# Optimization experiments

Measured on AMD Instinct MI355X. Metric: run time of the kernel, lower is better.

The kernel has to match this reference:

```python
import jax, jax.numpy as jnp
import numpy as np
import math

D_MODEL = 1024
NUM_HEADS = 16
D_K = D_MODEL // NUM_HEADS
B, S = 2, 2048


def _linear_weight(key, out_f, in_f):
    return jax.random.normal(key, (out_f, in_f), jnp.float32) * math.sqrt(2.0 / in_f)


def setup_inputs() -> dict:
    key = jax.random.key(0)
    ks = jax.random.split(key, 5)
    x = jax.random.normal(ks[0], (B, S, D_MODEL), jnp.float32)
    return {
        "x": x,
        "Wq": _linear_weight(ks[1], D_MODEL, D_MODEL),
        "bq": jnp.zeros((D_MODEL,), jnp.float32),
        "Wk": _linear_weight(ks[2], D_MODEL, D_MODEL),
        "bk": jnp.zeros((D_MODEL,), jnp.float32),
        "Wv": _linear_weight(ks[3], D_MODEL, D_MODEL),
        "bv": jnp.zeros((D_MODEL,), jnp.float32),
        "Wo": _linear_weight(ks[4], D_MODEL, D_MODEL),
        "bo": jnp.zeros((D_MODEL,), jnp.float32),
    }


def reference(x, Wq, bq, Wk, bk, Wv, bv, Wo, bo):
    b, s, _ = x.shape
    # Projections: x @ W.T + b (CustomLinear stores weight as (out, in))
    q = jnp.einsum("bsd,ed->bse", x, Wq) + bq
    k = jnp.einsum("bsd,ed->bse", x, Wk) + bk
    v = jnp.einsum("bsd,ed->bse", x, Wv) + bv
    # (b, h, s, d_k)
    q = q.reshape(b, s, NUM_HEADS, D_K).transpose(0, 2, 1, 3)
    k = k.reshape(b, s, NUM_HEADS, D_K).transpose(0, 2, 1, 3)
    v = v.reshape(b, s, NUM_HEADS, D_K).transpose(0, 2, 1, 3)
    # Scaled dot-product attention with fully materialized scores (faithful)
    scores = jnp.einsum("bhqd,bhkd->bhqk", q, k) / math.sqrt(D_K)
    attn = jax.nn.softmax(scores, axis=-1)
    out = jnp.einsum("bhqk,bhkd->bhqd", attn, v)
    out = out.transpose(0, 2, 1, 3).reshape(b, s, D_MODEL)
    return jnp.einsum("bsd,ed->bse", out, Wo) + bo
```

## Files before the change

kernel.cpp:

```cpp
#include <hip/hip_runtime.h>
#include <hip/hip_bf16.h>

using bf16 = __hip_bfloat16;
typedef __attribute__((ext_vector_type(8))) short short8;
typedef __attribute__((ext_vector_type(4))) short s4v;
typedef __attribute__((ext_vector_type(4))) float float4v;
typedef __attribute__((ext_vector_type(4))) float f32x4;

#define MFMA16(a, b, c) __builtin_amdgcn_mfma_f32_16x16x32_bf16((a), (b), (c), 0, 0, 0)

#define GLD_LDS16(g, l)                                            \
    __builtin_amdgcn_global_load_lds(                              \
        (const __attribute__((address_space(1))) void*)(g),        \
        (__attribute__((address_space(3))) void*)(l), 16, 0, 0)

constexpr int Bc = 2;
constexpr int Sc = 2048;
constexpr int Hc = 16;
constexpr int DKc = 64;
constexpr int Dc = 1024;
constexpr size_t MEG = 1024 * 1024;

union BFU { bf16 h; short s; };

__device__ inline short bfbits(float f) {
    BFU u; u.h = __float2bfloat16(f); return u.s;
}

__device__ inline float bits2f(short s) {
    BFU u; u.s = s; return __bfloat162float(u.h);
}

__device__ inline short8 load_cvt8(const float* __restrict__ p) {
    f32x4 a = *(const f32x4*)p;
    f32x4 b = *(const f32x4*)(p + 4);
    short8 r;
    r[0] = bfbits(a[0]); r[1] = bfbits(a[1]); r[2] = bfbits(a[2]); r[3] = bfbits(a[3]);
    r[4] = bfbits(b[0]); r[5] = bfbits(b[1]); r[6] = bfbits(b[2]); r[7] = bfbits(b[3]);
    return r;
}

__global__ __launch_bounds__(256) void cvt_kernel(
    const float* __restrict__ x, const float* __restrict__ Wq,
    const float* __restrict__ Wk, const float* __restrict__ Wv,
    const float* __restrict__ Wo, bf16* __restrict__ dst)
{
    const size_t i = ((size_t)blockIdx.x * 256 + threadIdx.x) * 8;
    const float* s;
    if      (i < 4 * MEG) s = x  + i;
    else if (i < 5 * MEG) s = Wq + (i - 4 * MEG);
    else if (i < 6 * MEG) s = Wk + (i - 5 * MEG);
    else if (i < 7 * MEG) s = Wv + (i - 6 * MEG);
    else                  s = Wo + (i - 7 * MEG);
    *(short8*)(dst + i) = load_cvt8(s);
}

__global__ __launch_bounds__(256) void qkv_gemm_kernel(
    const bf16* __restrict__ x,
    const bf16* __restrict__ Wq, const float* __restrict__ bq,
    const bf16* __restrict__ Wk, const float* __restrict__ bk,
    const bf16* __restrict__ Wv, const float* __restrict__ bv,
    bf16* __restrict__ q_ws, bf16* __restrict__ k_ws, bf16* __restrict__ v_ws)
{
    constexpr int BM = 128, BN = 128, BK = 32;
    __shared__ __align__(16) bf16 sA[BM * BK];
    __shared__ __align__(16) bf16 sB[BN * BK];

    const int bx = blockIdx.x;
    const int sel = bx >> 3;
    const int n0 = (bx & 7) * BN;
    const int m0 = blockIdx.y * BM;

    const bf16* __restrict__ Wsel = (sel == 0) ? Wq : ((sel == 1) ? Wk : Wv);
    const float* __restrict__ bsel = (sel == 0) ? bq : ((sel == 1) ? bk : bv);

    const int t = threadIdx.x;
    const int lane = t & 63;
    const int wave = t >> 6;
    const int ln = lane & 15;
    const int qd = lane >> 4;
    const int wm = (wave >> 1) * 64;
    const int wn = (wave & 1) * 64;

    const int gr = lane >> 2;
    const int gc = (lane & 3) * 8;

    float4v acc[4][4];
#pragma unroll
    for (int i = 0; i < 4; i++)
#pragma unroll
        for (int j = 0; j < 4; j++) acc[i][j] = (float4v)0.0f;

    for (int kk = 0; kk < Dc; kk += BK) {
        __syncthreads();
#pragma unroll
        for (int cc = 0; cc < 2; cc++) {
            const int c = wave * 2 + cc;
            GLD_LDS16(x    + (size_t)(m0 + c * 16 + gr) * Dc + kk + gc, &sA[c * 512]);
            GLD_LDS16(Wsel + (size_t)(n0 + c * 16 + gr) * Dc + kk + gc, &sB[c * 512]);
        }
        __syncthreads();

        short8 af[4], wf[4];
#pragma unroll
        for (int i = 0; i < 4; i++)
            af[i] = *(const short8*)&sA[(wm + i * 16 + ln) * BK + qd * 8];
#pragma unroll
        for (int j = 0; j < 4; j++)
            wf[j] = *(const short8*)&sB[(wn + j * 16 + ln) * BK + qd * 8];
#pragma unroll
        for (int i = 0; i < 4; i++)
#pragma unroll
            for (int j = 0; j < 4; j++)
                acc[i][j] = MFMA16(af[i], wf[j], acc[i][j]);
    }

    constexpr float QSCALE = 0.125f * 1.44269504088896f;

#pragma unroll
    for (int j = 0; j < 4; j++) {
        const int n = n0 + wn + j * 16 + ln;
        const float bias = bsel[n];
        const int h_ = n >> 6, d_ = n & 63;
#pragma unroll
        for (int i = 0; i < 4; i++) {
            const int mbase = m0 + wm + i * 16 + qd * 4;
            if (sel == 2) {
                const int b_ = mbase >> 11, s_ = mbase & 2047;
                s4v pk;
#pragma unroll
                for (int r = 0; r < 4; r++)
                    pk[r] = bfbits(acc[i][j][r] + bias);
                *(s4v*)&v_ws[(((size_t)(b_ * Hc + h_)) * DKc + d_) * Sc + s_] = pk;
            } else {
#pragma unroll
                for (int r = 0; r < 4; r++) {
                    const int m = mbase + r;
                    const int b_ = m >> 11, s_ = m & 2047;
                    float v = acc[i][j][r] + bias;
                    if (sel == 0) v *= QSCALE;
                    const bf16 o = __float2bfloat16(v);
                    if (sel == 0)
                        q_ws[(((size_t)(b_ * Hc + h_)) * Sc + s_) * DKc + d_] = o;
                    else
                        k_ws[(((size_t)(b_ * Hc + h_)) * Sc + s_) * DKc + d_] = o;
                }
            }
        }
    }
}

__global__ __launch_bounds__(512, 6) void attn_kernel(
    const bf16* __restrict__ q_ws, const bf16* __restrict__ k_ws,
    const bf16* __restrict__ v_ws, bf16* __restrict__ po0,
    bf16* __restrict__ po1, float* __restrict__ l_ws)
{
    constexpr int LQP = 76;
    constexpr int NKT = 16;
    __shared__ __align__(16) bf16 sK[2][64 * 64];
    __shared__ __align__(16) bf16 sV[2][64 * 64];
    __shared__ __align__(16) short sP[8][16 * LQP];

    const int bh = blockIdx.x;
    const int qt = blockIdx.y;
    const int sp = blockIdx.z;
    const int t = threadIdx.x;
    const int lane = t & 63;
    const int wave = t >> 6;
    const int ln = lane & 15;
    const int qd = lane >> 4;
    short* const sPw = sP[wave];

    const bf16* __restrict__ Qbase = q_ws + (size_t)bh * Sc * DKc + qt * 128 * DKc;
    const bf16* __restrict__ Kbase = k_ws + ((size_t)bh * Sc + sp * 1024) * DKc;
    const bf16* __restrict__ Vbase = v_ws + (size_t)bh * DKc * Sc + sp * 1024;

    const int rloc = lane >> 3;
    const int blk = lane & 7;

    short8 qf[2];
#pragma unroll
    for (int ks = 0; ks < 2; ks++)
        qf[ks] = *(const short8*)
            (Qbase + (size_t)(wave * 16 + ln) * DKc + ks * 32 + qd * 8);

    {
        const int row = wave * 8 + rloc;
        const int gb = blk ^ (row & 7);
        GLD_LDS16(Kbase + (size_t)row * DKc + gb * 8, &sK[0][wave * 512]);
        GLD_LDS16(Vbase + (size_t)row * Sc + gb * 8, &sV[0][wave * 512]);
    }

    short8 ones8;
    {
        const short ob = (ln == 0) ? (short)0x3F80 : (short)0;
#pragma unroll
        for (int i = 0; i < 8; i++) ones8[i] = ob;
    }

    float4v oacc[5];
#pragma unroll
    for (int j = 0; j < 5; j++) oacc[j] = (float4v)0.0f;

    for (int kt = 0; kt < NKT; kt++) {
        const int cur = kt & 1;
        __syncthreads();
        if (kt + 1 < NKT) {
            const int nxt = (kt + 1) & 1;
            const int row = wave * 8 + rloc;
            const int gb = blk ^ (row & 7);
            GLD_LDS16(Kbase + (size_t)((kt + 1) * 64 + row) * DKc + gb * 8,
                      &sK[nxt][wave * 512]);
            GLD_LDS16(Vbase + (size_t)row * Sc + (kt + 1) * 64 + gb * 8,
                      &sV[nxt][wave * 512]);
        }

        float4v sacc[4];
#pragma unroll
        for (int j = 0; j < 4; j++) sacc[j] = (float4v)0.0f;
        __builtin_amdgcn_s_setprio(1);
#pragma unroll
        for (int ks = 0; ks < 2; ks++) {
#pragma unroll
            for (int j = 0; j < 4; j++) {
                const int row = j * 16 + ln;
                const short8 ak = *(const short8*)
                    &sK[cur][row * 64 + (((ks * 4 + qd) ^ (row & 7)) << 3)];
                sacc[j] = MFMA16(ak, qf[ks], sacc[j]);
            }
        }
        __builtin_amdgcn_s_setprio(0);

#pragma unroll
        for (int j = 0; j < 4; j++) {
            s4v pk;
#pragma unroll
            for (int r = 0; r < 4; r++)
                pk[r] = bfbits(exp2f(sacc[j][r]));
            *(s4v*)&sPw[ln * LQP + j * 16 + qd * 4] = pk;
        }

        __builtin_amdgcn_s_setprio(1);
#pragma unroll
        for (int ks = 0; ks < 2; ks++) {
            const s4v p0 = *(const s4v*)&sPw[ln * LQP + ks * 32 + qd * 8];
            const s4v p1 = *(const s4v*)&sPw[ln * LQP + ks * 32 + qd * 8 + 4];
            const short8 ap = __builtin_shufflevector(p0, p1, 0, 1, 2, 3, 4, 5, 6, 7);
#pragma unroll
            for (int j = 0; j < 4; j++) {
                const int row = j * 16 + ln;
                const short8 bv_ = *(const short8*)
                    &sV[cur][row * 64 + (((ks * 4 + qd) ^ (row & 7)) << 3)];
                oacc[j] = MFMA16(ap, bv_, oacc[j]);
            }
            oacc[4] = MFMA16(ap, ones8, oacc[4]);
        }
        __builtin_amdgcn_s_setprio(0);
    }

    const int b_ = bh >> 4, h_ = bh & 15;
    bf16* __restrict__ po = sp ? po1 : po0;
    if (ln == 0) {
#pragma unroll
        for (int r = 0; r < 4; r++)
            l_ws[(size_t)(sp * 32 + bh) * Sc + qt * 128 + wave * 16 + qd * 4 + r] =
                oacc[4][r];
    }
#pragma unroll
    for (int r = 0; r < 4; r++) {
        const float l = __shfl(oacc[4][r], lane & 48, 64);
        const float inv = 1.0f / l;
        const int s_ = qt * 128 + wave * 16 + qd * 4 + r;
#pragma unroll
        for (int j = 0; j < 4; j++) {
            const int d_ = j * 16 + ln;
            po[(((size_t)(b_ * Sc + s_)) * Hc + h_) * DKc + d_] =
                __float2bfloat16(oacc[j][r] * inv);
        }
    }
}

__global__ __launch_bounds__(256) void combine_kernel(
    bf16* po0, const bf16* __restrict__ po1, const float* __restrict__ l_ws)
{
    const size_t gid = (size_t)blockIdx.x * 256 + threadIdx.x;
    const size_t e = gid * 8;
    const int flat = (int)(e >> 6);
    const int h_ = flat & 15;
    const int bs = flat >> 4;
    const int b_ = bs >> 11, s_ = bs & 2047;
    const int bh = b_ * Hc + h_;
    const float l0 = l_ws[(size_t)bh * Sc + s_];
    const float l1 = l_ws[(size_t)(32 + bh) * Sc + s_];
    const float inv = 1.0f / (l0 + l1);
    const float w0 = l0 * inv, w1 = l1 * inv;
    const short8 a = *(const short8*)(po0 + e);
    const short8 b = *(const short8*)(po1 + e);
    short8 o;
#pragma unroll
    for (int i = 0; i < 8; i++)
        o[i] = bfbits(bits2f(a[i]) * w0 + bits2f(b[i]) * w1);
    *(short8*)(po0 + e) = o;
}

__global__ __launch_bounds__(256) void out_gemm_kernel(
    const bf16* __restrict__ A, const bf16* __restrict__ Wo,
    const float* __restrict__ bo, float* __restrict__ out)
{
    constexpr int BM = 128, BN = 128, BK = 32;
    __shared__ __align__(16) bf16 sA[BM * BK];
    __shared__ __align__(16) bf16 sB[BN * BK];

    const int n0 = blockIdx.x * BN;
    const int m0 = blockIdx.y * BM;

    const int t = threadIdx.x;
    const int lane = t & 63;
    const int wave = t >> 6;
    const int ln = lane & 15;
    const int qd = lane >> 4;
    const int wm = (wave >> 1) * 64;
    const int wn = (wave & 1) * 64;

    const int gr = lane >> 2;
    const int gc = (lane & 3) * 8;

    float4v acc[4][4];
#pragma unroll
    for (int i = 0; i < 4; i++)
#pragma unroll
        for (int j = 0; j < 4; j++) acc[i][j] = (float4v)0.0f;

    for (int kk = 0; kk < Dc; kk += BK) {
        __syncthreads();
#pragma unroll
        for (int cc = 0; cc < 2; cc++) {
            const int c = wave * 2 + cc;
            GLD_LDS16(A  + (size_t)(m0 + c * 16 + gr) * Dc + kk + gc, &sA[c * 512]);
            GLD_LDS16(Wo + (size_t)(n0 + c * 16 + gr) * Dc + kk + gc, &sB[c * 512]);
        }
        __syncthreads();

        short8 af[4], wf[4];
#pragma unroll
        for (int i = 0; i < 4; i++)
            af[i] = *(const short8*)&sA[(wm + i * 16 + ln) * BK + qd * 8];
#pragma unroll
        for (int j = 0; j < 4; j++)
            wf[j] = *(const short8*)&sB[(wn + j * 16 + ln) * BK + qd * 8];
#pragma unroll
        for (int i = 0; i < 4; i++)
#pragma unroll
            for (int j = 0; j < 4; j++)
                acc[i][j] = MFMA16(af[i], wf[j], acc[i][j]);
    }

#pragma unroll
    for (int j = 0; j < 4; j++) {
        const int n = n0 + wn + j * 16 + ln;
        const float bias = bo[n];
#pragma unroll
        for (int i = 0; i < 4; i++) {
            const int mbase = m0 + wm + i * 16 + qd * 4;
#pragma unroll
            for (int r = 0; r < 4; r++) {
                const int m = mbase + r;
                out[(size_t)m * Dc + n] = acc[i][j][r] + bias;
            }
        }
    }
}

extern "C" void kernel_launch(void* const* d_in, const int* in_sizes, int n_in,
                              void* d_out, int out_size, void* d_ws, size_t ws_size,
                              hipStream_t stream)
{
    const float* x  = (const float*)d_in[0];
    const float* Wq = (const float*)d_in[1];
    const float* bq = (const float*)d_in[2];
    const float* Wk = (const float*)d_in[3];
    const float* bk = (const float*)d_in[4];
    const float* Wv = (const float*)d_in[5];
    const float* bv = (const float*)d_in[6];
    const float* Wo = (const float*)d_in[7];
    const float* bo = (const float*)d_in[8];
    float* out = (float*)d_out;

    bf16* base  = (bf16*)d_ws;
    bf16* q_ws  = base;
    bf16* k_ws  = base + 4 * MEG;
    bf16* v_ws  = base + 8 * MEG;
    bf16* ao_ws = base + 12 * MEG;
    bf16* xb    = base + 16 * MEG;
    bf16* po1   = xb;
    bf16* wqb   = base + 20 * MEG;
    float* l_ws = (float*)wqb;
    bf16* wkb   = base + 21 * MEG;
    bf16* wvb   = base + 22 * MEG;
    bf16* wob   = base + 23 * MEG;

    cvt_kernel<<<dim3(4096), 256, 0, stream>>>(x, Wq, Wk, Wv, Wo, xb);
    qkv_gemm_kernel<<<dim3(24, 32), 256, 0, stream>>>(
        xb, wqb, bq, wkb, bk, wvb, bv, q_ws, k_ws, v_ws);
    attn_kernel<<<dim3(32, 16, 2), 512, 0, stream>>>(
        q_ws, k_ws, v_ws, ao_ws, po1, l_ws);
    combine_kernel<<<dim3(2048), 256, 0, stream>>>(ao_ws, po1, l_ws);
    out_gemm_kernel<<<dim3(8, 32), 256, 0, stream>>>(ao_ws, wob, bo, out);
}
```

Before: 208.4 us.

## Switch attention to 32x32 MFMA with fragment-ordered K/V layout and register P

The attention kernel moves from 16x16x32 to 32x32x16 bf16 MFMA, with four waves of 32 query rows each instead of eight waves of 16. The QKV GEMM epilogue now writes K and V straight into MFMA-fragment order, so each tile can be staged into LDS with plain contiguous global_load_lds copies and read without swizzling. The P matrix no longer goes through LDS: it is packed with v_cvt_pk_bf16_f32 and rearranged across half-waves with lane shuffles. The aim is fewer LDS round trips and fewer MFMA issues per tile; the cost is scattered epilogue stores, more registers, and fewer threads per block.

```diff
diff --git a/kernel.cpp b/kernel.cpp
--- a/kernel.cpp
+++ b/kernel.cpp
@@ -6,8 +6,11 @@
 typedef __attribute__((ext_vector_type(4))) short s4v;
 typedef __attribute__((ext_vector_type(4))) float float4v;
 typedef __attribute__((ext_vector_type(4))) float f32x4;
+typedef __attribute__((ext_vector_type(16))) float f32x16;
+typedef __attribute__((ext_vector_type(4))) int i32x4;
 
 #define MFMA16(a, b, c) __builtin_amdgcn_mfma_f32_16x16x32_bf16((a), (b), (c), 0, 0, 0)
+#define MFMA32(a, b, c) __builtin_amdgcn_mfma_f32_32x32x16_bf16((a), (b), (c), 0, 0, 0)
 
 #define GLD_LDS16(g, l)                                            \
     __builtin_amdgcn_global_load_lds(                              \
@@ -22,6 +25,7 @@
 constexpr size_t MEG = 1024 * 1024;
 
 union BFU { bf16 h; short s; };
+union PKU { i32x4 i; short8 s; };
 
 __device__ inline short bfbits(float f) {
     BFU u; u.h = __float2bfloat16(f); return u.s;
@@ -29,6 +33,12 @@
 
 __device__ inline float bits2f(short s) {
     BFU u; u.s = s; return __bfloat162float(u.h);
+}
+
+__device__ inline unsigned cvtpk(float a, float b) {
+    unsigned r;
+    asm("v_cvt_pk_bf16_f32 %0, %1, %2" : "=v"(r) : "v"(a), "v"(b));
+    return r;
 }
 
 __device__ inline short8 load_cvt8(const float* __restrict__ p) {
@@ -125,41 +135,47 @@
 #pragma unroll
         for (int i = 0; i < 4; i++) {
             const int mbase = m0 + wm + i * 16 + qd * 4;
+            const int b_ = mbase >> 11, s0_ = mbase & 2047;
             if (sel == 2) {
-                const int b_ = mbase >> 11, s_ = mbase & 2047;
+                const int dv_ = d_ >> 5, cV = d_ & 31;
+                const int ktg = s0_ >> 6, ksl = (s0_ >> 4) & 3;
+                const int hiV = (s0_ >> 3) & 1, i0 = s0_ & 7;
                 s4v pk;
 #pragma unroll
                 for (int r = 0; r < 4; r++)
                     pk[r] = bfbits(acc[i][j][r] + bias);
-                *(s4v*)&v_ws[(((size_t)(b_ * Hc + h_)) * DKc + d_) * Sc + s_] = pk;
+                *(s4v*)&v_ws[(size_t)(b_ * Hc + h_) * Sc * DKc + ktg * 4096
+                             + (dv_ * 4 + ksl) * 512 + (cV + 32 * hiV) * 8 + i0] = pk;
+            } else if (sel == 1) {
+                const int ks_ = d_ >> 4, hiK = (d_ >> 3) & 1, ii = d_ & 7;
+#pragma unroll
+                for (int r = 0; r < 4; r++) {
+                    const int s_ = s0_ + r;
+                    const int ktg = s_ >> 6, kv = (s_ >> 5) & 1, cK = s_ & 31;
+                    k_ws[(size_t)(b_ * Hc + h_) * Sc * DKc + ktg * 4096
+                         + (kv * 4 + ks_) * 512 + (cK + 32 * hiK) * 8 + ii] =
+                        __float2bfloat16(acc[i][j][r] + bias);
+                }
             } else {
 #pragma unroll
                 for (int r = 0; r < 4; r++) {
-                    const int m = mbase + r;
-                    const int b_ = m >> 11, s_ = m & 2047;
-                    float v = acc[i][j][r] + bias;
-                    if (sel == 0) v *= QSCALE;
-                    const bf16 o = __float2bfloat16(v);
-                    if (sel == 0)
-                        q_ws[(((size_t)(b_ * Hc + h_)) * Sc + s_) * DKc + d_] = o;
-                    else
-                        k_ws[(((size_t)(b_ * Hc + h_)) * Sc + s_) * DKc + d_] = o;
+                    const int s_ = s0_ + r;
+                    q_ws[(((size_t)(b_ * Hc + h_)) * Sc + s_) * DKc + d_] =
+                        __float2bfloat16((acc[i][j][r] + bias) * QSCALE);
                 }
             }
         }
     }
 }
 
-__global__ __launch_bounds__(512, 6) void attn_kernel(
-    const bf16* __restrict__ q_ws, const bf16* __restrict__ k_ws,
-    const bf16* __restrict__ v_ws, bf16* __restrict__ po0,
+__global__ __launch_bounds__(256, 4) void attn_kernel(
+    const bf16* __restrict__ q_ws, const bf16* __restrict__ kf_ws,
+    const bf16* __restrict__ vf_ws, bf16* __restrict__ po0,
     bf16* __restrict__ po1, float* __restrict__ l_ws)
 {
-    constexpr int LQP = 76;
     constexpr int NKT = 16;
-    __shared__ __align__(16) bf16 sK[2][64 * 64];
-    __shared__ __align__(16) bf16 sV[2][64 * 64];
-    __shared__ __align__(16) short sP[8][16 * LQP];
+    __shared__ __align__(16) bf16 sK[2][8 * 512];
+    __shared__ __align__(16) bf16 sV[2][8 * 512];
 
     const int bh = blockIdx.x;
     const int qt = blockIdx.y;
@@ -167,116 +183,116 @@
     const int t = threadIdx.x;
     const int lane = t & 63;
     const int wave = t >> 6;
-    const int ln = lane & 15;
-    const int qd = lane >> 4;
-    short* const sPw = sP[wave];
-
-    const bf16* __restrict__ Qbase = q_ws + (size_t)bh * Sc * DKc + qt * 128 * DKc;
-    const bf16* __restrict__ Kbase = k_ws + ((size_t)bh * Sc + sp * 1024) * DKc;
-    const bf16* __restrict__ Vbase = v_ws + (size_t)bh * DKc * Sc + sp * 1024;
-
-    const int rloc = lane >> 3;
-    const int blk = lane & 7;
-
-    short8 qf[2];
-#pragma unroll
-    for (int ks = 0; ks < 2; ks++)
-        qf[ks] = *(const short8*)
-            (Qbase + (size_t)(wave * 16 + ln) * DKc + ks * 32 + qd * 8);
-
-    {
-        const int row = wave * 8 + rloc;
-        const int gb = blk ^ (row & 7);
-        GLD_LDS16(Kbase + (size_t)row * DKc + gb * 8, &sK[0][wave * 512]);
-        GLD_LDS16(Vbase + (size_t)row * Sc + gb * 8, &sV[0][wave * 512]);
-    }
+    const int c = lane & 31;
+    const int hi = lane >> 5;
+
+    const bf16* __restrict__ Qbase = q_ws + (size_t)bh * Sc * DKc
+                                   + (size_t)(qt * 128 + wave * 32) * DKc;
+    const bf16* __restrict__ KF = kf_ws + ((size_t)bh * Sc + sp * 1024) * DKc;
+    const bf16* __restrict__ VF = vf_ws + ((size_t)bh * Sc + sp * 1024) * DKc;
+
+    short8 qf[4];
+#pragma unroll
+    for (int ks = 0; ks < 4; ks++)
+        qf[ks] = *(const short8*)(Qbase + (size_t)c * DKc + ks * 16 + hi * 8);
 
     short8 ones8;
     {
-        const short ob = (ln == 0) ? (short)0x3F80 : (short)0;
+        const short ob = (c == 0) ? (short)0x3F80 : (short)0;
 #pragma unroll
         for (int i = 0; i < 8; i++) ones8[i] = ob;
     }
 
-    float4v oacc[5];
-#pragma unroll
-    for (int j = 0; j < 5; j++) oacc[j] = (float4v)0.0f;
+    auto stage = [&](int buf, int kt2) {
+#pragma unroll
+        for (int cc = 0; cc < 4; cc++) {
+            const int cid = (wave << 2) + cc;
+            if (cid < 8)
+                GLD_LDS16(KF + (size_t)kt2 * 4096 + cid * 512 + lane * 8,
+                          &sK[buf][cid * 512]);
+            else
+                GLD_LDS16(VF + (size_t)kt2 * 4096 + (cid - 8) * 512 + lane * 8,
+                          &sV[buf][(cid - 8) * 512]);
+        }
+    };
+
+    f32x16 oacc0 = (f32x16)0.0f;
+    f32x16 oacc1 = (f32x16)0.0f;
+    f32x16 den   = (f32x16)0.0f;
+
+    stage(0, 0);
 
     for (int kt = 0; kt < NKT; kt++) {
         const int cur = kt & 1;
         __syncthreads();
-        if (kt + 1 < NKT) {
-            const int nxt = (kt + 1) & 1;
-            const int row = wave * 8 + rloc;
-            const int gb = blk ^ (row & 7);
-            GLD_LDS16(Kbase + (size_t)((kt + 1) * 64 + row) * DKc + gb * 8,
-                      &sK[nxt][wave * 512]);
-            GLD_LDS16(Vbase + (size_t)row * Sc + (kt + 1) * 64 + gb * 8,
-                      &sV[nxt][wave * 512]);
-        }
-
-        float4v sacc[4];
-#pragma unroll
-        for (int j = 0; j < 4; j++) sacc[j] = (float4v)0.0f;
-        __builtin_amdgcn_s_setprio(1);
-#pragma unroll
-        for (int ks = 0; ks < 2; ks++) {
-#pragma unroll
-            for (int j = 0; j < 4; j++) {
-                const int row = j * 16 + ln;
-                const short8 ak = *(const short8*)
-                    &sK[cur][row * 64 + (((ks * 4 + qd) ^ (row & 7)) << 3)];
-                sacc[j] = MFMA16(ak, qf[ks], sacc[j]);
+        if (kt + 1 < NKT) stage(cur ^ 1, kt + 1);
+
+#pragma unroll
+        for (int kv = 0; kv < 2; kv++) {
+            f32x16 sacc = (f32x16)0.0f;
+            __builtin_amdgcn_s_setprio(1);
+#pragma unroll
+            for (int ks = 0; ks < 4; ks++) {
+                const short8 kfr = *(const short8*)
+                    &sK[cur][(kv * 4 + ks) * 512 + lane * 8];
+                sacc = MFMA32(kfr, qf[ks], sacc);
             }
-        }
-        __builtin_amdgcn_s_setprio(0);
-
-#pragma unroll
-        for (int j = 0; j < 4; j++) {
-            s4v pk;
-#pragma unroll
-            for (int r = 0; r < 4; r++)
-                pk[r] = bfbits(exp2f(sacc[j][r]));
-            *(s4v*)&sPw[ln * LQP + j * 16 + qd * 4] = pk;
-        }
-
-        __builtin_amdgcn_s_setprio(1);
-#pragma unroll
-        for (int ks = 0; ks < 2; ks++) {
-            const s4v p0 = *(const s4v*)&sPw[ln * LQP + ks * 32 + qd * 8];
-            const s4v p1 = *(const s4v*)&sPw[ln * LQP + ks * 32 + qd * 8 + 4];
-            const short8 ap = __builtin_shufflevector(p0, p1, 0, 1, 2, 3, 4, 5, 6, 7);
-#pragma unroll
-            for (int j = 0; j < 4; j++) {
-                const int row = j * 16 + ln;
-                const short8 bv_ = *(const short8*)
-                    &sV[cur][row * 64 + (((ks * 4 + qd) ^ (row & 7)) << 3)];
-                oacc[j] = MFMA16(ap, bv_, oacc[j]);
+            __builtin_amdgcn_s_setprio(0);
+
+            unsigned s0[4][2], sw[4][2];
+#pragma unroll
+            for (int q = 0; q < 4; q++)
+#pragma unroll
+                for (int j = 0; j < 2; j++)
+                    s0[q][j] = cvtpk(exp2f(sacc[q * 4 + j * 2]),
+                                     exp2f(sacc[q * 4 + j * 2 + 1]));
+#pragma unroll
+            for (int q = 0; q < 4; q++)
+#pragma unroll
+                for (int j = 0; j < 2; j++)
+                    sw[q][j] = (unsigned)__shfl_xor((int)s0[q][j], 32, 64);
+
+            __builtin_amdgcn_s_setprio(1);
+#pragma unroll
+            for (int m = 0; m < 2; m++) {
+                PKU u;
+                u.i[0] = (int)(hi ? sw[2 * m + 1][0] : s0[2 * m][0]);
+                u.i[1] = (int)(hi ? sw[2 * m + 1][1] : s0[2 * m][1]);
+                u.i[2] = (int)(hi ? s0[2 * m + 1][0] : sw[2 * m][0]);
+                u.i[3] = (int)(hi ? s0[2 * m + 1][1] : sw[2 * m][1]);
+                const short8 ap = u.s;
+                const int ksl = kv * 2 + m;
+                const short8 vf0 = *(const short8*)
+                    &sV[cur][(0 + ksl) * 512 + lane * 8];
+                const short8 vf1 = *(const short8*)
+                    &sV[cur][(4 + ksl) * 512 + lane * 8];
+                oacc0 = MFMA32(ap, vf0, oacc0);
+                oacc1 = MFMA32(ap, vf1, oacc1);
+                den   = MFMA32(ap, ones8, den);
             }
-            oacc[4] = MFMA16(ap, ones8, oacc[4]);
-        }
-        __builtin_amdgcn_s_setprio(0);
+            __builtin_amdgcn_s_setprio(0);
+        }
     }
 
     const int b_ = bh >> 4, h_ = bh & 15;
     bf16* __restrict__ po = sp ? po1 : po0;
-    if (ln == 0) {
-#pragma unroll
-        for (int r = 0; r < 4; r++)
-            l_ws[(size_t)(sp * 32 + bh) * Sc + qt * 128 + wave * 16 + qd * 4 + r] =
-                oacc[4][r];
-    }
-#pragma unroll
-    for (int r = 0; r < 4; r++) {
-        const float l = __shfl(oacc[4][r], lane & 48, 64);
+    if (c == 0) {
+#pragma unroll
+        for (int r = 0; r < 16; r++) {
+            const int qrow = (r & 3) + 8 * (r >> 2) + 4 * hi;
+            l_ws[(size_t)(sp * 32 + bh) * Sc + qt * 128 + wave * 32 + qrow] =
+                den[r];
+        }
+    }
+#pragma unroll
+    for (int r = 0; r < 16; r++) {
+        const float l = __shfl(den[r], lane & 32, 64);
         const float inv = 1.0f / l;
-        const int s_ = qt * 128 + wave * 16 + qd * 4 + r;
-#pragma unroll
-        for (int j = 0; j < 4; j++) {
-            const int d_ = j * 16 + ln;
-            po[(((size_t)(b_ * Sc + s_)) * Hc + h_) * DKc + d_] =
-                __float2bfloat16(oacc[j][r] * inv);
-        }
+        const int qrow = (r & 3) + 8 * (r >> 2) + 4 * hi;
+        const int s_ = qt * 128 + wave * 32 + qrow;
+        const size_t rowb = (((size_t)(b_ * Sc + s_)) * Hc + h_) * DKc;
+        po[rowb + c]      = __float2bfloat16(oacc0[r] * inv);
+        po[rowb + 32 + c] = __float2bfloat16(oacc1[r] * inv);
     }
 }
 
@@ -402,7 +418,7 @@
     cvt_kernel<<<dim3(4096), 256, 0, stream>>>(x, Wq, Wk, Wv, Wo, xb);
     qkv_gemm_kernel<<<dim3(24, 32), 256, 0, stream>>>(
         xb, wqb, bq, wkb, bk, wvb, bv, q_ws, k_ws, v_ws);
-    attn_kernel<<<dim3(32, 16, 2), 512, 0, stream>>>(
+    attn_kernel<<<dim3(32, 16, 2), 256, 0, stream>>>(
         q_ws, k_ws, v_ws, ao_ws, po1, l_ws);
     combine_kernel<<<dim3(2048), 256, 0, stream>>>(ao_ws, po1, l_ws);
     out_gemm_kernel<<<dim3(8, 32), 256, 0, stream>>>(ao_ws, wob, bo, out);
```

Result: no change. 211.6 us (+1.5%).
